# Optimization experiments

Measured on AMD Instinct MI355X. Metric: run time of the kernel, lower is better.

## Reference

```python
import jax, jax.numpy as jnp
import numpy as np

O, C_IN, P, D = 256, 256, 96, 2
KH, KW = 51, 51


def setup_inputs() -> dict:
    key = jax.random.key(0)
    k1, k2, k3 = jax.random.split(key, 3)
    # coordinate grid in [-1, 1], shape (1, D, KH, KW) like a normalized meshgrid
    ys = jnp.linspace(-1.0, 1.0, KH, dtype=jnp.float32)
    xs = jnp.linspace(-1.0, 1.0, KW, dtype=jnp.float32)
    gy, gx = jnp.meshgrid(ys, xs, indexing="ij")
    x = jnp.stack([gy, gx], axis=0)[None]  # (1, 2, KH, KW)
    # learned point coordinates, trunc-normal-ish in [-1, 1]
    weight_coord = jnp.clip(0.3 * jax.random.normal(k1, (O, P, D), dtype=jnp.float32), -1.0, 1.0)
    # per-point radius, initialized to init_radius
    radius = jnp.full((O, P, 1, 1), 0.5, dtype=jnp.float32)
    # point weights
    weights = 0.02 * jax.random.normal(k2, (O, C_IN, P), dtype=jnp.float32)
    return {"x": x, "weight_coord": weight_coord, "radius": radius, "weights": weights}


def reference(x, weight_coord, radius, weights):
    o, p, d = weight_coord.shape
    spatial = x.shape[2:]  # (KH, KW)
    n = int(np.prod(spatial))
    coords = x.reshape(d, n).T  # (N, D)
    # broadcast coord diff + L1 distance over dim_linear: (O, P, N)
    dist = jnp.sum(jnp.abs(weight_coord[:, :, None, :] - coords[None, None, :, :]), axis=-1)
    # triangular basis
    vals = jax.nn.relu(1.0 - dist / radius.reshape(o, p, 1))  # (O, P, N)
    # count of points covering each location, used to normalize
    count = jnp.sum(vals != 0, axis=1, keepdims=True)  # (O, 1, N), int
    weighted = vals / (count.astype(vals.dtype) + 1e-6)
    # batched small matmul over points: (O, C_in, P) @ (O, P, N) -> (O, C_in, N)
    kernels = jnp.einsum("ocp,opn->ocn", weights, weighted)
    kernels = kernels.reshape(o, weights.shape[1], *spatial)
    # dim_linear == 2 branch: transpose last two dims, flip along dim 2
    kernels = jnp.flip(jnp.swapaxes(kernels, -2, -1), axis=2)
    return kernels
```

## Files before the change

### kernel.cpp

```cpp
#include <hip/hip_runtime.h>

#define O_DIM 256
#define C_DIM 256
#define P_DIM 96
#define KHW 51
#define NSP 2601
#define RPITCH 1044
#define PHW 1024

typedef __attribute__((ext_vector_type(8))) short short8v;
typedef __attribute__((ext_vector_type(4))) float float4v;
typedef __attribute__((ext_vector_type(4), aligned(16))) float float4a;
typedef __attribute__((ext_vector_type(4), aligned(4))) float float4u;

static __device__ __forceinline__ unsigned f2bf(float f) {
  union { float f; unsigned u; } v; v.f = f;
  return (v.u + 0x7FFFu + ((v.u >> 16) & 1u)) >> 16;
}
static __device__ __forceinline__ unsigned cvtpk(float lo, float hi) {
  unsigned r;
  asm("v_cvt_pk_bf16_f32 %0, %1, %2" : "=v"(r) : "v"(lo), "v"(hi));
  return r;
}
static __device__ __forceinline__ float bcast(unsigned u) {
  union { unsigned u; float f; } v; v.u = u; return v.f;
}
static __device__ __forceinline__ void barrier_lgkm() {
  asm volatile("s_waitcnt lgkmcnt(0)" ::: "memory");
  __builtin_amdgcn_s_barrier();
}

__global__ __launch_bounds__(1024, 1) void smp_fused(
    const float* __restrict__ xg,
    const float* __restrict__ wc,
    const float* __restrict__ rad,
    const float* __restrict__ wts,
    float* __restrict__ out)
{
  __shared__ float Ylds[52];
  __shared__ __align__(16) float pyL[96], pxL[96], prL[96];
  __shared__ __align__(16) unsigned short RBuf[64 * RPITCH];

  const int b = blockIdx.x;
  const int o = b >> 2;
  const int cq = b & 3;
  const int tid = threadIdx.x;
  const int wave = tid >> 6;
  const int lane = tid & 63;
  const int row16 = lane & 15;
  const int kgrp = lane >> 4;

  if (tid < 51) Ylds[tid] = xg[tid * KHW];
  if (tid < 96) {
    pyL[tid] = wc[((size_t)o * P_DIM + tid) * 2];
    pxL[tid] = wc[((size_t)o * P_DIM + tid) * 2 + 1];
    prL[tid] = 1.0f / rad[(size_t)o * P_DIM + tid];
  }

  short8v wfr[4][3];
  {
    const float* Wo = wts + ((size_t)o * C_DIM + cq * 64) * P_DIM;
#pragma unroll
    for (int mf = 0; mf < 4; ++mf) {
      const float* src = Wo + (mf * 16 + row16) * P_DIM;
#pragma unroll
      for (int ks = 0; ks < 3; ++ks) {
        const float4 a4 = *(const float4*)(src + ks * 32 + kgrp * 8);
        const float4 c4 = *(const float4*)(src + ks * 32 + kgrp * 8 + 4);
        short8v f;
        f[0] = (short)f2bf(a4.x); f[1] = (short)f2bf(a4.y);
        f[2] = (short)f2bf(a4.z); f[3] = (short)f2bf(a4.w);
        f[4] = (short)f2bf(c4.x); f[5] = (short)f2bf(c4.y);
        f[6] = (short)f2bf(c4.z); f[7] = (short)f2bf(c4.w);
        wfr[mf][ks] = f;
      }
    }
  }
  __syncthreads();

  const size_t obase = ((size_t)o * C_DIM + cq * 64) * NSP;

  for (int p = 0; p < 3; ++p) {
    const int base = p * PHW;
    const int width = (p < 2) ? PHW : (NSP - 2 * PHW);
    const int ntiles = (p < 2) ? 64 : 35;

    for (int t = wave; t < ntiles; t += 16) {
      const int jlc = t * 16 + row16;
      const int jl = base + jlc;
      const int jc = jl < NSP ? jl : NSP - 1;
      const int i = jc / KHW;
      const int jj = jc - i * KHW;
      const float gy = Ylds[jj];
      const float gx = Ylds[50 - i];

      float4v acc[4];
#pragma unroll
      for (int mf = 0; mf < 4; ++mf) acc[mf] = (float4v){0.f, 0.f, 0.f, 0.f};
      int cnt = 0;

#pragma unroll
      for (int ks = 0; ks < 3; ++ks) {
        const int pb = ks * 32 + kgrp * 8;
        const float4a py0 = *(const float4a*)&pyL[pb];
        const float4a py1 = *(const float4a*)&pyL[pb + 4];
        const float4a px0 = *(const float4a*)&pxL[pb];
        const float4a px1 = *(const float4a*)&pxL[pb + 4];
        const float4a pr0 = *(const float4a*)&prL[pb];
        const float4a pr1 = *(const float4a*)&prL[pb + 4];
        float s[8], v[8];
#pragma unroll
        for (int j = 0; j < 4; ++j) {
          s[j]     = fmaf(fabsf(py0[j] - gy) + fabsf(px0[j] - gx), -pr0[j], 1.0f);
          s[j + 4] = fmaf(fabsf(py1[j] - gy) + fabsf(px1[j] - gx), -pr1[j], 1.0f);
        }
#pragma unroll
        for (int j = 0; j < 8; ++j) {
          v[j] = s[j] > 0.0f ? s[j] : 0.0f;
          cnt += (s[j] > 0.0f);
        }
        union { unsigned u[4]; short8v sv; } bfr;
#pragma unroll
        for (int jp = 0; jp < 4; ++jp) bfr.u[jp] = cvtpk(v[2 * jp], v[2 * jp + 1]);
#pragma unroll
        for (int mf = 0; mf < 4; ++mf)
          acc[mf] = __builtin_amdgcn_mfma_f32_16x16x32_bf16(
              wfr[mf][ks], bfr.sv, acc[mf], 0, 0, 0);
      }
      cnt += __shfl_xor(cnt, 16);
      cnt += __shfl_xor(cnt, 32);
      const float inv = __builtin_amdgcn_rcpf((float)cnt + 1e-6f);

      if (jl < NSP) {
#pragma unroll
        for (int mf = 0; mf < 4; ++mf)
#pragma unroll
          for (int r2 = 0; r2 < 4; ++r2)
            RBuf[(mf * 16 + kgrp * 4 + r2) * RPITCH + jlc] =
                (unsigned short)f2bf(acc[mf][r2] * inv);
      }
    }
    barrier_lgkm();

#pragma unroll
    for (int k2 = 0; k2 < 4; ++k2) {
      const int row = wave * 4 + k2;
      const unsigned short* rb = &RBuf[row * RPITCH];
      float* gp = out + obase + (size_t)row * NSP + base;
      for (int it = 0; it < width / 256; ++it) {
        const int j = it * 256 + lane * 4;
        const uint2 u = *(const uint2*)&rb[j];
        float4u v = {bcast(u.x << 16), bcast(u.x & 0xFFFF0000u),
                     bcast(u.y << 16), bcast(u.y & 0xFFFF0000u)};
        __builtin_nontemporal_store(v, (float4u*)(gp + j));
      }
      if (width & 255) {
        const int j = (width & ~255) + lane * 4;
        if (j + 4 <= width) {
          const uint2 u = *(const uint2*)&rb[j];
          float4u v = {bcast(u.x << 16), bcast(u.x & 0xFFFF0000u),
                       bcast(u.y << 16), bcast(u.y & 0xFFFF0000u)};
          __builtin_nontemporal_store(v, (float4u*)(gp + j));
        } else if (j < width) {
#pragma unroll
          for (int r2 = 0; r2 < 4; ++r2)
            if (j + r2 < width) gp[j + r2] = bcast(((unsigned)rb[j + r2]) << 16);
        }
      }
    }
    barrier_lgkm();
  }
}

extern "C" void kernel_launch(void* const* d_in, const int* in_sizes, int n_in,
                              void* d_out, int out_size, void* d_ws, size_t ws_size,
                              hipStream_t stream) {
  const float* xg  = (const float*)d_in[0];
  const float* wcp = (const float*)d_in[1];
  const float* rad = (const float*)d_in[2];
  const float* wts = (const float*)d_in[3];
  float* out = (float*)d_out;
  hipLaunchKernelGGL(smp_fused, dim3(O_DIM * 4), dim3(1024), 0, stream,
                     xg, wcp, rad, wts, out);
}
```

Before: 226.8 us.

## Halve phase width and stage weights in LDS to fit more blocks per CU

Each block now processes the output in six 512-column phases instead of three 1024-column ones, which halves the LDS result buffer. The bf16 weight fragments are kept in a padded LDS array instead of 12 registers per lane. The launch bounds ask for more resident blocks, so compute phases of one block can overlap the streaming stores of another. Software bf16 rounding is replaced with the packed hardware convert. The trade-offs are extra LDS reads of weights inside the MFMA loop, more barriers per block, a small last phase that leaves most waves idle, and a tighter register budget that could cause spills.

New measurement: 222.8 us. Within noise of the previous version (-1.8%).

```diff
diff --git a/kernel.cpp b/kernel.cpp
--- a/kernel.cpp
+++ b/kernel.cpp
@@ -5,18 +5,16 @@
 #define P_DIM 96
 #define KHW 51
 #define NSP 2601
-#define RPITCH 1044
-#define PHW 1024
+#define PHW 512
+#define NPH 6
+#define RPITCH 520
+#define WPITCH 104
 
 typedef __attribute__((ext_vector_type(8))) short short8v;
 typedef __attribute__((ext_vector_type(4))) float float4v;
 typedef __attribute__((ext_vector_type(4), aligned(16))) float float4a;
 typedef __attribute__((ext_vector_type(4), aligned(4))) float float4u;
 
-static __device__ __forceinline__ unsigned f2bf(float f) {
-  union { float f; unsigned u; } v; v.f = f;
-  return (v.u + 0x7FFFu + ((v.u >> 16) & 1u)) >> 16;
-}
 static __device__ __forceinline__ unsigned cvtpk(float lo, float hi) {
   unsigned r;
   asm("v_cvt_pk_bf16_f32 %0, %1, %2" : "=v"(r) : "v"(lo), "v"(hi));
@@ -30,7 +28,7 @@
   __builtin_amdgcn_s_barrier();
 }
 
-__global__ __launch_bounds__(1024, 1) void smp_fused(
+__global__ __launch_bounds__(1024, 8) void smp_fused(
     const float* __restrict__ xg,
     const float* __restrict__ wc,
     const float* __restrict__ rad,
@@ -39,6 +37,7 @@
 {
   __shared__ float Ylds[52];
   __shared__ __align__(16) float pyL[96], pxL[96], prL[96];
+  __shared__ __align__(16) unsigned short Wlds[64 * WPITCH];
   __shared__ __align__(16) unsigned short RBuf[64 * RPITCH];
 
   const int b = blockIdx.x;
@@ -56,34 +55,24 @@
     pxL[tid] = wc[((size_t)o * P_DIM + tid) * 2 + 1];
     prL[tid] = 1.0f / rad[(size_t)o * P_DIM + tid];
   }
-
-  short8v wfr[4][3];
   {
     const float* Wo = wts + ((size_t)o * C_DIM + cq * 64) * P_DIM;
-#pragma unroll
-    for (int mf = 0; mf < 4; ++mf) {
-      const float* src = Wo + (mf * 16 + row16) * P_DIM;
-#pragma unroll
-      for (int ks = 0; ks < 3; ++ks) {
-        const float4 a4 = *(const float4*)(src + ks * 32 + kgrp * 8);
-        const float4 c4 = *(const float4*)(src + ks * 32 + kgrp * 8 + 4);
-        short8v f;
-        f[0] = (short)f2bf(a4.x); f[1] = (short)f2bf(a4.y);
-        f[2] = (short)f2bf(a4.z); f[3] = (short)f2bf(a4.w);
-        f[4] = (short)f2bf(c4.x); f[5] = (short)f2bf(c4.y);
-        f[6] = (short)f2bf(c4.z); f[7] = (short)f2bf(c4.w);
-        wfr[mf][ks] = f;
-      }
+    for (int idx = tid; idx < 64 * 48; idx += 1024) {
+      const int row = idx / 48;
+      const int col = (idx - row * 48) * 2;
+      const float a0 = Wo[row * P_DIM + col];
+      const float a1 = Wo[row * P_DIM + col + 1];
+      *(unsigned*)&Wlds[row * WPITCH + col] = cvtpk(a0, a1);
     }
   }
   __syncthreads();
 
   const size_t obase = ((size_t)o * C_DIM + cq * 64) * NSP;
 
-  for (int p = 0; p < 3; ++p) {
+  for (int p = 0; p < NPH; ++p) {
     const int base = p * PHW;
-    const int width = (p < 2) ? PHW : (NSP - 2 * PHW);
-    const int ntiles = (p < 2) ? 64 : 35;
+    const int width = (p < NPH - 1) ? PHW : (NSP - (NPH - 1) * PHW);
+    const int ntiles = (width + 15) >> 4;
 
     for (int t = wave; t < ntiles; t += 16) {
       const int jlc = t * 16 + row16;
@@ -102,43 +91,36 @@
 #pragma unroll
       for (int ks = 0; ks < 3; ++ks) {
         const int pb = ks * 32 + kgrp * 8;
-        const float4a py0 = *(const float4a*)&pyL[pb];
-        const float4a py1 = *(const float4a*)&pyL[pb + 4];
-        const float4a px0 = *(const float4a*)&pxL[pb];
-        const float4a px1 = *(const float4a*)&pxL[pb + 4];
-        const float4a pr0 = *(const float4a*)&prL[pb];
-        const float4a pr1 = *(const float4a*)&prL[pb + 4];
-        float s[8], v[8];
+        union { unsigned u[4]; short8v sv; } bfr;
 #pragma unroll
-        for (int j = 0; j < 4; ++j) {
-          s[j]     = fmaf(fabsf(py0[j] - gy) + fabsf(px0[j] - gx), -pr0[j], 1.0f);
-          s[j + 4] = fmaf(fabsf(py1[j] - gy) + fabsf(px1[j] - gx), -pr1[j], 1.0f);
+        for (int h = 0; h < 2; ++h) {
+          const float4a py = *(const float4a*)&pyL[pb + h * 4];
+          const float4a px = *(const float4a*)&pxL[pb + h * 4];
+          const float4a pr = *(const float4a*)&prL[pb + h * 4];
+          float s0 = fmaf(fabsf(py[0] - gy) + fabsf(px[0] - gx), -pr[0], 1.0f);
+          float s1 = fmaf(fabsf(py[1] - gy) + fabsf(px[1] - gx), -pr[1], 1.0f);
+          float s2 = fmaf(fabsf(py[2] - gy) + fabsf(px[2] - gx), -pr[2], 1.0f);
+          float s3 = fmaf(fabsf(py[3] - gy) + fabsf(px[3] - gx), -pr[3], 1.0f);
+          cnt += (s0 > 0.0f) + (s1 > 0.0f) + (s2 > 0.0f) + (s3 > 0.0f);
+          bfr.u[h * 2]     = cvtpk(s0 > 0.0f ? s0 : 0.0f, s1 > 0.0f ? s1 : 0.0f);
+          bfr.u[h * 2 + 1] = cvtpk(s2 > 0.0f ? s2 : 0.0f, s3 > 0.0f ? s3 : 0.0f);
         }
 #pragma unroll
-        for (int j = 0; j < 8; ++j) {
-          v[j] = s[j] > 0.0f ? s[j] : 0.0f;
-          cnt += (s[j] > 0.0f);
+        for (int mf = 0; mf < 4; ++mf) {
+          const short8v afr = *(const short8v*)&Wlds[(mf * 16 + row16) * WPITCH + pb];
+          acc[mf] = __builtin_amdgcn_mfma_f32_16x16x32_bf16(afr, bfr.sv, acc[mf], 0, 0, 0);
         }
-        union { unsigned u[4]; short8v sv; } bfr;
-#pragma unroll
-        for (int jp = 0; jp < 4; ++jp) bfr.u[jp] = cvtpk(v[2 * jp], v[2 * jp + 1]);
-#pragma unroll
-        for (int mf = 0; mf < 4; ++mf)
-          acc[mf] = __builtin_amdgcn_mfma_f32_16x16x32_bf16(
-              wfr[mf][ks], bfr.sv, acc[mf], 0, 0, 0);
       }
       cnt += __shfl_xor(cnt, 16);
       cnt += __shfl_xor(cnt, 32);
       const float inv = __builtin_amdgcn_rcpf((float)cnt + 1e-6f);
 
-      if (jl < NSP) {
 #pragma unroll
-        for (int mf = 0; mf < 4; ++mf)
+      for (int mf = 0; mf < 4; ++mf)
 #pragma unroll
-          for (int r2 = 0; r2 < 4; ++r2)
-            RBuf[(mf * 16 + kgrp * 4 + r2) * RPITCH + jlc] =
-                (unsigned short)f2bf(acc[mf][r2] * inv);
-      }
+        for (int r2 = 0; r2 < 4; ++r2)
+          RBuf[(mf * 16 + kgrp * 4 + r2) * RPITCH + jlc] =
+              (unsigned short)cvtpk(acc[mf][r2] * inv, 0.0f);
     }
     barrier_lgkm();
 
@@ -155,7 +137,7 @@
         __builtin_nontemporal_store(v, (float4u*)(gp + j));
       }
       if (width & 255) {
-        const int j = (width & ~255) + lane * 4;
+        const int j = lane * 4;
         if (j + 4 <= width) {
           const uint2 u = *(const uint2*)&rb[j];
           float4u v = {bcast(u.x << 16), bcast(u.x & 0xFFFF0000u),
```
